# Performance work log

Measured on AMD Instinct MI355X. Metric: run time of the kernel, lower is better.

## Reference

```python
import jax, jax.numpy as jnp
import numpy as np

N = 33554432  # number of elements
POS_WEIGHT = 1.0
NEG_WEIGHT = 8.0
EPS = 1e-07


def setup_inputs() -> dict:
    key = jax.random.key(0)
    k1, k2 = jax.random.split(key)
    outputs = jax.random.uniform(k1, (N,), dtype=jnp.float32)  # probabilities in (0,1)
    targets = jax.random.randint(k2, (N,), 0, 2, dtype=jnp.int32)  # binary labels
    return {"outputs": outputs, "targets": targets}


def reference(outputs, targets):
    # weight-select, log, and mean-reduction in one fused elementwise pass
    pos = POS_WEIGHT * -jnp.log(outputs + EPS)
    neg = NEG_WEIGHT * -jnp.log(1.0 - outputs + EPS)
    loss = jnp.where(targets == 1, pos, neg)
    return jnp.mean(loss)
```

## Files before the change

kernel.cpp:

```cpp
#include <hip/hip_runtime.h>

#define NEG_W 8.0f
#define EPS 1e-7f
#define TPB 256
#define VPT 4
#define BLOCKS 8192

__global__ __launch_bounds__(TPB) void bce_partial(
    const float4* __restrict__ out4, const int4* __restrict__ tgt4,
    float* __restrict__ partials) {
  const int base = blockIdx.x * (TPB * VPT) + threadIdx.x;

  float4 o[VPT];
  int4 t[VPT];
#pragma unroll
  for (int u = 0; u < VPT; ++u) {
    const int idx = base + u * TPB;
    o[u] = out4[idx];
    t[u] = tgt4[idx];
  }
  __builtin_amdgcn_sched_barrier(0);

  float acc0 = 0.0f, acc1 = 0.0f, acc2 = 0.0f, acc3 = 0.0f;
#pragma unroll
  for (int u = 0; u < VPT; ++u) {
    float x0 = (t[u].x == 1) ? (o[u].x + EPS) : (1.0f - o[u].x + EPS);
    float w0 = (t[u].x == 1) ? 1.0f : NEG_W;
    float x1 = (t[u].y == 1) ? (o[u].y + EPS) : (1.0f - o[u].y + EPS);
    float w1 = (t[u].y == 1) ? 1.0f : NEG_W;
    float x2 = (t[u].z == 1) ? (o[u].z + EPS) : (1.0f - o[u].z + EPS);
    float w2 = (t[u].z == 1) ? 1.0f : NEG_W;
    float x3 = (t[u].w == 1) ? (o[u].w + EPS) : (1.0f - o[u].w + EPS);
    float w3 = (t[u].w == 1) ? 1.0f : NEG_W;
    acc0 = fmaf(w0, __logf(x0), acc0);
    acc1 = fmaf(w1, __logf(x1), acc1);
    acc2 = fmaf(w2, __logf(x2), acc2);
    acc3 = fmaf(w3, __logf(x3), acc3);
  }
  float sum = -((acc0 + acc1) + (acc2 + acc3));

  for (int off = 32; off > 0; off >>= 1)
    sum += __shfl_down(sum, off, 64);

  __shared__ float wsum[TPB / 64];
  const int lane = threadIdx.x & 63;
  const int wid = threadIdx.x >> 6;
  if (lane == 0) wsum[wid] = sum;
  __syncthreads();
  if (threadIdx.x == 0) {
    float s = 0.0f;
    for (int w = 0; w < TPB / 64; ++w) s += wsum[w];
    partials[blockIdx.x] = s;
  }
}

__global__ __launch_bounds__(TPB) void bce_finalize(
    const float* __restrict__ partials, float* __restrict__ out, int nblocks,
    double inv_n) {
  double s = 0.0;
  for (int i = threadIdx.x; i < nblocks; i += TPB) s += (double)partials[i];
  for (int off = 32; off > 0; off >>= 1)
    s += __shfl_down(s, off, 64);
  __shared__ double wsum[TPB / 64];
  const int lane = threadIdx.x & 63;
  const int wid = threadIdx.x >> 6;
  if (lane == 0) wsum[wid] = s;
  __syncthreads();
  if (threadIdx.x == 0) {
    double tot = 0.0;
    for (int w = 0; w < TPB / 64; ++w) tot += wsum[w];
    out[0] = (float)(tot * inv_n);
  }
}

extern "C" void kernel_launch(void* const* d_in, const int* in_sizes, int n_in,
                              void* d_out, int out_size, void* d_ws, size_t ws_size,
                              hipStream_t stream) {
  const float4* out4 = (const float4*)d_in[0];
  const int4* tgt4 = (const int4*)d_in[1];
  const int n = in_sizes[0];
  float* partials = (float*)d_ws;
  (void)n;

  bce_partial<<<BLOCKS, TPB, 0, stream>>>(out4, tgt4, partials);
  bce_finalize<<<1, TPB, 0, stream>>>(partials, (float*)d_out, BLOCKS,
                                      1.0 / (double)33554432);
}
```

Baseline: 276.4 us.

## Stream inputs through double-buffered LDS via async global_load_lds with persistent blocks

Replaces the one-shot per-block register loads with a persistent grid of 512 blocks. Each block loops over 16 rounds and prefetches the next round directly into LDS with global_load_lds while computing the current one. Manual vmcnt waits keep one round of loads in flight, aiming to keep the memory system busy and cut block launch and tail overhead. The risks are lower occupancy from only two blocks per CU and reliance on hand-written waitcnt ordering without barriers.

```diff
diff --git a/kernel.cpp b/kernel.cpp
--- a/kernel.cpp
+++ b/kernel.cpp
@@ -1,42 +1,78 @@
 #include <hip/hip_runtime.h>
+#include <stdint.h>
 
 #define NEG_W 8.0f
 #define EPS 1e-7f
 #define TPB 256
-#define VPT 4
-#define BLOCKS 8192
+#define GRID 512
+#define ROUNDS 16
+#define F4R (TPB * 4)
+#define F4B (F4R * ROUNDS)
+
+typedef const __attribute__((address_space(1))) void* gp_t;
+typedef __attribute__((address_space(3))) void* lp_t;
+
+#define WAIT8() asm volatile("s_waitcnt vmcnt(8)" ::: "memory")
+#define WAIT0() asm volatile("s_waitcnt vmcnt(0)" ::: "memory")
+#define CFENCE() asm volatile("" ::: "memory")
 
 __global__ __launch_bounds__(TPB) void bce_partial(
     const float4* __restrict__ out4, const int4* __restrict__ tgt4,
     float* __restrict__ partials) {
-  const int base = blockIdx.x * (TPB * VPT) + threadIdx.x;
+  __shared__ float4 sf[2][F4R];
+  __shared__ int4 si[2][F4R];
 
-  float4 o[VPT];
-  int4 t[VPT];
-#pragma unroll
-  for (int u = 0; u < VPT; ++u) {
-    const int idx = base + u * TPB;
-    o[u] = out4[idx];
-    t[u] = tgt4[idx];
-  }
-  __builtin_amdgcn_sched_barrier(0);
+  const int tid = threadIdx.x;
+  const long base = (long)blockIdx.x * F4B + tid;
+  const float4* po = out4 + base;
+  const int4* pt = tgt4 + base;
+
+#define ISSUE(r, buf)                                                       \
+  do {                                                                      \
+    _Pragma("unroll")                                                       \
+    for (int j = 0; j < 4; ++j) {                                           \
+      __builtin_amdgcn_global_load_lds((gp_t)(po + (r)*F4R + j * TPB),      \
+                                       (lp_t)&sf[buf][j * TPB + tid], 16,   \
+                                       0, 0);                               \
+      __builtin_amdgcn_global_load_lds((gp_t)(pt + (r)*F4R + j * TPB),      \
+                                       (lp_t)&si[buf][j * TPB + tid], 16,   \
+                                       0, 0);                               \
+    }                                                                       \
+  } while (0)
 
   float acc0 = 0.0f, acc1 = 0.0f, acc2 = 0.0f, acc3 = 0.0f;
+
+  ISSUE(0, 0);
 #pragma unroll
-  for (int u = 0; u < VPT; ++u) {
-    float x0 = (t[u].x == 1) ? (o[u].x + EPS) : (1.0f - o[u].x + EPS);
-    float w0 = (t[u].x == 1) ? 1.0f : NEG_W;
-    float x1 = (t[u].y == 1) ? (o[u].y + EPS) : (1.0f - o[u].y + EPS);
-    float w1 = (t[u].y == 1) ? 1.0f : NEG_W;
-    float x2 = (t[u].z == 1) ? (o[u].z + EPS) : (1.0f - o[u].z + EPS);
-    float w2 = (t[u].z == 1) ? 1.0f : NEG_W;
-    float x3 = (t[u].w == 1) ? (o[u].w + EPS) : (1.0f - o[u].w + EPS);
-    float w3 = (t[u].w == 1) ? 1.0f : NEG_W;
-    acc0 = fmaf(w0, __logf(x0), acc0);
-    acc1 = fmaf(w1, __logf(x1), acc1);
-    acc2 = fmaf(w2, __logf(x2), acc2);
-    acc3 = fmaf(w3, __logf(x3), acc3);
+  for (int r = 0; r < ROUNDS; ++r) {
+    const int buf = r & 1;
+    if (r + 1 < ROUNDS) {
+      ISSUE(r + 1, buf ^ 1);
+      WAIT8();
+    } else {
+      WAIT0();
+    }
+#pragma unroll
+    for (int j = 0; j < 4; ++j) {
+      float4 o = sf[buf][j * TPB + tid];
+      int4 t = si[buf][j * TPB + tid];
+      float x0 = (t.x == 1) ? (o.x + EPS) : (1.0f - o.x + EPS);
+      float w0 = (t.x == 1) ? 1.0f : NEG_W;
+      float x1 = (t.y == 1) ? (o.y + EPS) : (1.0f - o.y + EPS);
+      float w1 = (t.y == 1) ? 1.0f : NEG_W;
+      float x2 = (t.z == 1) ? (o.z + EPS) : (1.0f - o.z + EPS);
+      float w2 = (t.z == 1) ? 1.0f : NEG_W;
+      float x3 = (t.w == 1) ? (o.w + EPS) : (1.0f - o.w + EPS);
+      float w3 = (t.w == 1) ? 1.0f : NEG_W;
+      acc0 = fmaf(w0, __logf(x0), acc0);
+      acc1 = fmaf(w1, __logf(x1), acc1);
+      acc2 = fmaf(w2, __logf(x2), acc2);
+      acc3 = fmaf(w3, __logf(x3), acc3);
+    }
+    CFENCE();
   }
+#undef ISSUE
+
   float sum = -((acc0 + acc1) + (acc2 + acc3));
 
   for (int off = 32; off > 0; off >>= 1)
@@ -78,11 +114,9 @@
                               hipStream_t stream) {
   const float4* out4 = (const float4*)d_in[0];
   const int4* tgt4 = (const int4*)d_in[1];
-  const int n = in_sizes[0];
   float* partials = (float*)d_ws;
-  (void)n;
 
-  bce_partial<<<BLOCKS, TPB, 0, stream>>>(out4, tgt4, partials);
-  bce_finalize<<<1, TPB, 0, stream>>>(partials, (float*)d_out, BLOCKS,
+  bce_partial<<<GRID, TPB, 0, stream>>>(out4, tgt4, partials);
+  bce_finalize<<<1, TPB, 0, stream>>>(partials, (float*)d_out, GRID,
                                       1.0 / (double)33554432);
 }
```

After: 277.1 us. About the same (+0.3%).
